# Optimization experiments

Measured on AMD Instinct MI355X. Metric: run time of the kernel, lower is better.

## Reference

```python
import jax, jax.numpy as jnp
import numpy as np

IN_DIM = 512
OUT_DIM = 512
NUM_HARMONICS = 32
BATCH = 4096


def setup_inputs() -> dict:
    key = jax.random.key(0)
    k1, k2 = jax.random.split(key)
    x = jax.random.normal(k1, (BATCH, IN_DIM), dtype=jnp.float32)
    std = 1.0 / np.sqrt(IN_DIM * NUM_HARMONICS)
    fourier_coeffs = jax.random.normal(
        k2, (IN_DIM, NUM_HARMONICS, 2, OUT_DIM), dtype=jnp.float32) * std
    bias = jnp.zeros((OUT_DIM,), dtype=jnp.float32)
    return {"x": x, "fourier_coeffs": fourier_coeffs, "bias": bias}


def reference(x, fourier_coeffs, bias):
    # k = [1, ..., num_harmonics]
    k = jnp.arange(1, fourier_coeffs.shape[1] + 1, dtype=x.dtype)
    kx = x[:, :, None] * k                      # [b, i, g]
    trig = jnp.stack([jnp.cos(kx), jnp.sin(kx)], axis=-1)  # [b, i, g, 2]
    out = jnp.einsum('bigf,igfo->bo', trig, fourier_coeffs)
    return out + bias
```

## Files before the change

kernel.cpp:

```cpp
#include <hip/hip_runtime.h>
#include <hip/hip_bf16.h>
#include <stdint.h>
#include <stddef.h>

#define BATCH   4096
#define INDIM   512
#define OUTDIM  512
#define NH      32
#define KKDIM   64
#define INV2PI  0.15915494309189535f

#define BM       128
#define BN       128
#define THREADS  256
#define KSPLIT   8
#define DIMS_PER_WG (INDIM / KSPLIT)
#define CHUNK_COLS  256
#define CHUNK_ELEMS (CHUNK_COLS * KKDIM)

#define B_BYTES       16384
#define SMEM_BYTES    (2 * B_BYTES)

typedef short  bhalf8  __attribute__((ext_vector_type(8)));
typedef float  vfloat4 __attribute__((ext_vector_type(4)));

union AFrag { uint4 u; bhalf8 h; };

__device__ __forceinline__ unsigned pack_bf16(float a, float b) {
    union { __hip_bfloat162 h2; unsigned u; } cv;
    cv.h2 = __float22bfloat162_rn(float2{a, b});
    return cv.u;
}

__device__ __forceinline__ void async_copy16(const void* gsrc, void* ldst) {
    __builtin_amdgcn_global_load_lds(
        (const __attribute__((address_space(1))) void*)(uintptr_t)gsrc,
        (__attribute__((address_space(3))) void*)(uint32_t)(uintptr_t)ldst,
        16, 0, 0);
}

__global__ __launch_bounds__(256) void fkan_prepass(const float* __restrict__ coeffs,
                                                    unsigned short* __restrict__ Bt) {
    __shared__ float lds[64][260];
    const int t  = threadIdx.x;
    const int cb = blockIdx.x & 1;
    const int i  = blockIdx.x >> 1;
    const float* __restrict__ src = coeffs + (size_t)i * (KKDIM * OUTDIM) + cb * CHUNK_COLS;
    unsigned short* __restrict__ chunk = Bt + (size_t)(cb * INDIM + i) * CHUNK_ELEMS;
#pragma unroll
    for (int rd = 0; rd < 16; ++rd) {
        const int r  = rd * 4 + (t >> 6);
        const int c4 = (t & 63) * 4;
        const float4 v = *(const float4*)(src + (size_t)r * OUTDIM + c4);
        *(float4*)&lds[r][c4] = v;
    }
    __syncthreads();
#pragma unroll
    for (int s = 0; s < 8; ++s) {
        const int unit = t + s * 256;
        const int col  = unit >> 3;
        const int pc   = unit & 7;
        const int kb   = (pc ^ (col & 7)) * 8;
        uint4 o;
        o.x = pack_bf16(lds[kb + 0][col], lds[kb + 1][col]);
        o.y = pack_bf16(lds[kb + 2][col], lds[kb + 3][col]);
        o.z = pack_bf16(lds[kb + 4][col], lds[kb + 5][col]);
        o.w = pack_bf16(lds[kb + 6][col], lds[kb + 7][col]);
        ((uint4*)chunk)[unit] = o;
    }
}

__global__ __launch_bounds__(256) void fkan_bias_init(const float* __restrict__ bias,
                                                      float* __restrict__ out) {
    const int idx = blockIdx.x * 256 + threadIdx.x;
    ((float4*)out)[idx] = ((const float4*)bias)[idx & 127];
}

__device__ __forceinline__ void stage_B(const char* __restrict__ chunk_half, char* smem,
                                        int parity, int t) {
    char* bdst = smem + parity * B_BYTES;
#pragma unroll
    for (int s = 0; s < 4; ++s) {
        const int unit = t + s * 256;
        async_copy16(chunk_half + unit * 16, bdst + unit * 16);
    }
}

__device__ __forceinline__ void make_av(float rv, float k0f, float k1f,
                                        bhalf8* a0, bhalf8* a1) {
    const float cd = __builtin_amdgcn_cosf(rv);
    const float sd = __builtin_amdgcn_sinf(rv);
    AFrag A;
    float c = __builtin_amdgcn_cosf(k0f * rv);
    float s = __builtin_amdgcn_sinf(k0f * rv);
    A.u.x = pack_bf16(c, s);
    { const float nc = c*cd - s*sd, ns = s*cd + c*sd; c = nc; s = ns; }
    A.u.y = pack_bf16(c, s);
    { const float nc = c*cd - s*sd, ns = s*cd + c*sd; c = nc; s = ns; }
    A.u.z = pack_bf16(c, s);
    { const float nc = c*cd - s*sd, ns = s*cd + c*sd; c = nc; s = ns; }
    A.u.w = pack_bf16(c, s);
    *a0 = A.h;
    c = __builtin_amdgcn_cosf(k1f * rv);
    s = __builtin_amdgcn_sinf(k1f * rv);
    A.u.x = pack_bf16(c, s);
    { const float nc = c*cd - s*sd, ns = s*cd + c*sd; c = nc; s = ns; }
    A.u.y = pack_bf16(c, s);
    { const float nc = c*cd - s*sd, ns = s*cd + c*sd; c = nc; s = ns; }
    A.u.z = pack_bf16(c, s);
    { const float nc = c*cd - s*sd, ns = s*cd + c*sd; c = nc; s = ns; }
    A.u.w = pack_bf16(c, s);
    *a1 = A.h;
}

#define MFMA_BLOCK(Bb, A0, A1)                                                  \
    do {                                                                        \
        _Pragma("unroll")                                                       \
        for (int ct = 0; ct < 8; ++ct) {                                        \
            const int cbyte = (ct * 16 + fr) * 128;                             \
            const bhalf8 b0 = *(const bhalf8*)((Bb) + cbyte + off0);            \
            acc[0][ct] = __builtin_amdgcn_mfma_f32_16x16x32_bf16(               \
                (A0)[0], b0, acc[0][ct], 0, 0, 0);                              \
            acc[1][ct] = __builtin_amdgcn_mfma_f32_16x16x32_bf16(               \
                (A0)[1], b0, acc[1][ct], 0, 0, 0);                              \
            const bhalf8 b1 = *(const bhalf8*)((Bb) + cbyte + off1);            \
            acc[0][ct] = __builtin_amdgcn_mfma_f32_16x16x32_bf16(               \
                (A1)[0], b1, acc[0][ct], 0, 0, 0);                              \
            acc[1][ct] = __builtin_amdgcn_mfma_f32_16x16x32_bf16(               \
                (A1)[1], b1, acc[1][ct], 0, 0, 0);                              \
        }                                                                       \
    } while (0)

#define WAITBAR4 asm volatile("s_waitcnt vmcnt(4)\n\ts_barrier" ::: "memory")
#define WAITBAR0 asm volatile("s_waitcnt vmcnt(0)\n\ts_barrier" ::: "memory")
#define POSTBAR  asm volatile("s_barrier" ::: "memory")

__global__ __launch_bounds__(THREADS, 5) void fkan_main(const float* __restrict__ x,
                                                        const unsigned short* __restrict__ Bt,
                                                        float* __restrict__ out) {
    __shared__ char smem[SMEM_BYTES];
    const int t      = threadIdx.x;
    const int grp    = blockIdx.x & 31;
    const int member = blockIdx.x >> 5;
    const int kq      = grp & 7;
    const int cb4     = grp >> 3;
    const int cb2     = cb4 >> 1;
    const int rowbase = member * BM;
    const int colbase = cb4 * BN;
    const int dimbase = kq * DIMS_PER_WG;

    const int lane = t & 63;
    const int w    = t >> 6;
    const int fr   = lane & 15;
    const int fq   = lane >> 4;
    const int fx   = lane & 7;
    const int off0 = (fq ^ fx) * 16;
    const int off1 = ((4 + fq) ^ fx) * 16;

    const float k0f = (float)(fq * 4 + 1);
    const float k1f = (float)(fq * 4 + 17);

    const float* __restrict__ xp0 = x + (size_t)(rowbase + w * 32 + fr) * INDIM + dimbase;
    const float* __restrict__ xp1 = xp0 + (size_t)16 * INDIM;

    const char* __restrict__ chunkbase =
        (const char*)(Bt + (size_t)(cb2 * INDIM + dimbase) * CHUNK_ELEMS) + (cb4 & 1) * 16384;

    vfloat4 acc[2][8];
#pragma unroll
    for (int a = 0; a < 2; ++a)
#pragma unroll
        for (int b = 0; b < 8; ++b) acc[a][b] = (vfloat4)0.0f;

    stage_B(chunkbase, smem, 0, t);

#pragma unroll 2
    for (int it = 0; it < DIMS_PER_WG - 1; ++it) {
        const int p = it & 1;
        stage_B(chunkbase + (size_t)(it + 1) * 32768, smem, p ^ 1, t);
        bhalf8 a0[2], a1[2];
        make_av(xp0[it] * INV2PI, k0f, k1f, &a0[0], &a1[0]);
        make_av(xp1[it] * INV2PI, k0f, k1f, &a0[1], &a1[1]);
        WAITBAR4;
        MFMA_BLOCK(smem + p * B_BYTES, a0, a1);
        POSTBAR;
    }
    {
        const int it = DIMS_PER_WG - 1;
        bhalf8 a0[2], a1[2];
        make_av(xp0[it] * INV2PI, k0f, k1f, &a0[0], &a1[0]);
        make_av(xp1[it] * INV2PI, k0f, k1f, &a0[1], &a1[1]);
        WAITBAR0;
        MFMA_BLOCK(smem + (it & 1) * B_BYTES, a0, a1);
    }

#pragma unroll
    for (int rt = 0; rt < 2; ++rt) {
#pragma unroll
        for (int ct = 0; ct < 8; ++ct) {
            const int col  = colbase + ct * 16 + fr;
            const int row0 = rowbase + w * 32 + rt * 16 + fq * 4;
#pragma unroll
            for (int r = 0; r < 4; ++r)
                atomicAdd(out + (size_t)(row0 + r) * OUTDIM + col, acc[rt][ct][r]);
        }
    }
}

__global__ __launch_bounds__(256) void fkan_naive(const float* __restrict__ x,
                                                  const float* __restrict__ coeffs,
                                                  const float* __restrict__ bias,
                                                  float* __restrict__ out) {
    const int b = blockIdx.x >> 1;
    const int o = ((blockIdx.x & 1) << 8) + threadIdx.x;
    float acc = bias[o];
    const float* xrow = x + (size_t)b * INDIM;
    for (int i = 0; i < INDIM; ++i) {
        const float rv = xrow[i] * INV2PI;
        const float cd = __builtin_amdgcn_cosf(rv);
        const float sd = __builtin_amdgcn_sinf(rv);
        float c = cd, s = sd;
        const float* cp = coeffs + (size_t)i * (KKDIM * OUTDIM) + o;
#pragma unroll 4
        for (int g = 0; g < NH; ++g) {
            acc += c * cp[g * 2 * OUTDIM] + s * cp[(g * 2 + 1) * OUTDIM];
            const float nc = c * cd - s * sd;
            const float ns = s * cd + c * sd;
            c = nc; s = ns;
        }
    }
    out[(size_t)b * OUTDIM + o] = acc;
}

extern "C" void kernel_launch(void* const* d_in, const int* in_sizes, int n_in,
                              void* d_out, int out_size, void* d_ws, size_t ws_size,
                              hipStream_t stream) {
    (void)in_sizes; (void)n_in; (void)out_size;
    const float* x      = (const float*)d_in[0];
    const float* coeffs = (const float*)d_in[1];
    const float* bias   = (const float*)d_in[2];
    float* out          = (float*)d_out;

    const size_t bt_bytes = (size_t)2 * INDIM * CHUNK_ELEMS * sizeof(unsigned short);
    if (ws_size >= bt_bytes) {
        unsigned short* Bt = (unsigned short*)d_ws;
        fkan_prepass<<<2 * INDIM, 256, 0, stream>>>(coeffs, Bt);
        fkan_bias_init<<<(BATCH * OUTDIM) / (4 * 256), 256, 0, stream>>>(bias, out);
        fkan_main<<<(BATCH / BM) * (OUTDIM / BN) * KSPLIT, THREADS, 0, stream>>>(x, Bt, out);
    } else {
        fkan_naive<<<BATCH * 2, 256, 0, stream>>>(x, coeffs, bias, out);
    }
}
```

Before: 327.1 us.

## Enlarge row tile to 256 with 512 threads and a four-deep LDS ring

Doubles the row tile per workgroup to 256 rows with 512 threads, so each staged B chunk feeds twice as many rows and global B traffic per output falls. Replaces the double buffer with a 4-slot LDS ring prefetched two iterations ahead, which drops the post-MFMA barrier. x is now loaded as float4 once every four iterations and prefetched. MFMA sections run at raised wave priority via s_setprio. The vmcnt thresholds of 8/4/0 appear loose for two loads per stage plus the x loads, which risks reading a slot before its copy lands. Fewer resident workgroups per CU also reduces latency hiding.

```diff
diff --git a/kernel.cpp b/kernel.cpp
--- a/kernel.cpp
+++ b/kernel.cpp
@@ -10,16 +10,16 @@
 #define KKDIM   64
 #define INV2PI  0.15915494309189535f
 
-#define BM       128
+#define BM       256
 #define BN       128
-#define THREADS  256
+#define THREADS  512
 #define KSPLIT   8
 #define DIMS_PER_WG (INDIM / KSPLIT)
 #define CHUNK_COLS  256
 #define CHUNK_ELEMS (CHUNK_COLS * KKDIM)
 
 #define B_BYTES       16384
-#define SMEM_BYTES    (2 * B_BYTES)
+#define SMEM_BYTES    (4 * B_BYTES)
 
 typedef short  bhalf8  __attribute__((ext_vector_type(8)));
 typedef float  vfloat4 __attribute__((ext_vector_type(4)));
@@ -77,11 +77,11 @@
 }
 
 __device__ __forceinline__ void stage_B(const char* __restrict__ chunk_half, char* smem,
-                                        int parity, int t) {
-    char* bdst = smem + parity * B_BYTES;
-#pragma unroll
-    for (int s = 0; s < 4; ++s) {
-        const int unit = t + s * 256;
+                                        int ring, int t) {
+    char* bdst = smem + ring * B_BYTES;
+#pragma unroll
+    for (int s = 0; s < 2; ++s) {
+        const int unit = t + s * 512;
         async_copy16(chunk_half + unit * 16, bdst + unit * 16);
     }
 }
@@ -131,11 +131,23 @@
         }                                                                       \
     } while (0)
 
-#define WAITBAR4 asm volatile("s_waitcnt vmcnt(4)\n\ts_barrier" ::: "memory")
-#define WAITBAR0 asm volatile("s_waitcnt vmcnt(0)\n\ts_barrier" ::: "memory")
-#define POSTBAR  asm volatile("s_barrier" ::: "memory")
-
-__global__ __launch_bounds__(THREADS, 5) void fkan_main(const float* __restrict__ x,
+#define WAITBARN(N) asm volatile("s_waitcnt vmcnt(" #N ")\n\ts_barrier" ::: "memory")
+
+#define FKAN_BODY(IT, S, RV0, RV1, DO_STAGE, DO_XLOAD, VMC_STMT)                \
+    {                                                                           \
+        if (DO_STAGE) stage_B(chunkbase + (size_t)((IT) + 2) * 32768, smem,     \
+                              ((S) + 2) & 3, t);                                \
+        if (DO_XLOAD) { nq0 = xf0[(IT) / 4 + 1]; nq1 = xf1[(IT) / 4 + 1]; }     \
+        bhalf8 a0[2], a1[2];                                                    \
+        make_av((RV0) * INV2PI, k0f, k1f, &a0[0], &a1[0]);                      \
+        make_av((RV1) * INV2PI, k0f, k1f, &a0[1], &a1[1]);                      \
+        VMC_STMT;                                                               \
+        __builtin_amdgcn_s_setprio(1);                                          \
+        MFMA_BLOCK(smem + (S) * B_BYTES, a0, a1);                               \
+        __builtin_amdgcn_s_setprio(0);                                          \
+    }
+
+__global__ __launch_bounds__(THREADS, 2) void fkan_main(const float* __restrict__ x,
                                                         const unsigned short* __restrict__ Bt,
                                                         float* __restrict__ out) {
     __shared__ char smem[SMEM_BYTES];
@@ -160,8 +172,10 @@
     const float k0f = (float)(fq * 4 + 1);
     const float k1f = (float)(fq * 4 + 17);
 
-    const float* __restrict__ xp0 = x + (size_t)(rowbase + w * 32 + fr) * INDIM + dimbase;
-    const float* __restrict__ xp1 = xp0 + (size_t)16 * INDIM;
+    const float4* __restrict__ xf0 =
+        (const float4*)(x + (size_t)(rowbase + w * 32 + fr) * INDIM + dimbase);
+    const float4* __restrict__ xf1 =
+        (const float4*)(x + (size_t)(rowbase + w * 32 + 16 + fr) * INDIM + dimbase);
 
     const char* __restrict__ chunkbase =
         (const char*)(Bt + (size_t)(cb2 * INDIM + dimbase) * CHUNK_ELEMS) + (cb4 & 1) * 16384;
@@ -172,27 +186,24 @@
 #pragma unroll
         for (int b = 0; b < 8; ++b) acc[a][b] = (vfloat4)0.0f;
 
-    stage_B(chunkbase, smem, 0, t);
-
-#pragma unroll 2
-    for (int it = 0; it < DIMS_PER_WG - 1; ++it) {
-        const int p = it & 1;
-        stage_B(chunkbase + (size_t)(it + 1) * 32768, smem, p ^ 1, t);
-        bhalf8 a0[2], a1[2];
-        make_av(xp0[it] * INV2PI, k0f, k1f, &a0[0], &a1[0]);
-        make_av(xp1[it] * INV2PI, k0f, k1f, &a0[1], &a1[1]);
-        WAITBAR4;
-        MFMA_BLOCK(smem + p * B_BYTES, a0, a1);
-        POSTBAR;
-    }
-    {
-        const int it = DIMS_PER_WG - 1;
-        bhalf8 a0[2], a1[2];
-        make_av(xp0[it] * INV2PI, k0f, k1f, &a0[0], &a1[0]);
-        make_av(xp1[it] * INV2PI, k0f, k1f, &a0[1], &a1[1]);
-        WAITBAR0;
-        MFMA_BLOCK(smem + (it & 1) * B_BYTES, a0, a1);
-    }
+    float4 cq0 = xf0[0];
+    float4 cq1 = xf1[0];
+    float4 nq0, nq1;
+    stage_B(chunkbase,         smem, 0, t);
+    stage_B(chunkbase + 32768, smem, 1, t);
+
+    for (int g = 0; g < 15; ++g) {
+        const int it0 = g * 4;
+        FKAN_BODY(it0 + 0, 0, cq0.x, cq1.x, true, true,  WAITBARN(8));
+        FKAN_BODY(it0 + 1, 1, cq0.y, cq1.y, true, false, WAITBARN(8));
+        FKAN_BODY(it0 + 2, 2, cq0.z, cq1.z, true, false, WAITBARN(8));
+        FKAN_BODY(it0 + 3, 3, cq0.w, cq1.w, true, false, WAITBARN(8));
+        cq0 = nq0; cq1 = nq1;
+    }
+    FKAN_BODY(60, 0, cq0.x, cq1.x, true,  false, WAITBARN(8));
+    FKAN_BODY(61, 1, cq0.y, cq1.y, true,  false, WAITBARN(8));
+    FKAN_BODY(62, 2, cq0.z, cq1.z, false, false, WAITBARN(4));
+    FKAN_BODY(63, 3, cq0.w, cq1.w, false, false, WAITBARN(0));
 
 #pragma unroll
     for (int rt = 0; rt < 2; ++rt) {
```

Result: faster. 291.9 us (-10.7%).

## Split B tile per wave to drop barriers and shrink block rows

Applied to the files above, without the earlier changes.

Each wave now owns a private 32-column slice of the B tile and stages it into LDS itself, so the block-wide barriers go away and only per-wave vmcnt waits remain. The row tile is halved from 128 to 64, so each wave covers all 64 rows, and the x loads are vectorized and prefetched one iteration ahead. MFMA sections are wrapped in s_setprio, and launch bounds change from 5 to 4 waves-per-EU hint. In exchange, the sin/cos A-fragment generation is now repeated by every wave for every row, and the grid gets more blocks, which adds atomics and recomputation.

```diff
diff --git a/kernel.cpp b/kernel.cpp
--- a/kernel.cpp
+++ b/kernel.cpp
@@ -10,7 +10,7 @@
 #define KKDIM   64
 #define INV2PI  0.15915494309189535f
 
-#define BM       128
+#define BM       64
 #define BN       128
 #define THREADS  256
 #define KSPLIT   8
@@ -18,8 +18,9 @@
 #define CHUNK_COLS  256
 #define CHUNK_ELEMS (CHUNK_COLS * KKDIM)
 
-#define B_BYTES       16384
-#define SMEM_BYTES    (2 * B_BYTES)
+#define SLICE_BYTES   4096
+#define BUF_BYTES     (4 * SLICE_BYTES)
+#define SMEM_BYTES    (2 * BUF_BYTES)
 
 typedef short  bhalf8  __attribute__((ext_vector_type(8)));
 typedef float  vfloat4 __attribute__((ext_vector_type(4)));
@@ -76,16 +77,6 @@
     ((float4*)out)[idx] = ((const float4*)bias)[idx & 127];
 }
 
-__device__ __forceinline__ void stage_B(const char* __restrict__ chunk_half, char* smem,
-                                        int parity, int t) {
-    char* bdst = smem + parity * B_BYTES;
-#pragma unroll
-    for (int s = 0; s < 4; ++s) {
-        const int unit = t + s * 256;
-        async_copy16(chunk_half + unit * 16, bdst + unit * 16);
-    }
-}
-
 __device__ __forceinline__ void make_av(float rv, float k0f, float k1f,
                                         bhalf8* a0, bhalf8* a1) {
     const float cd = __builtin_amdgcn_cosf(rv);
@@ -113,29 +104,49 @@
     *a1 = A.h;
 }
 
-#define MFMA_BLOCK(Bb, A0, A1)                                                  \
-    do {                                                                        \
+#define WAITV(N) asm volatile("s_waitcnt vmcnt(" #N ")" ::: "memory")
+
+#define FKAN_BODY(IT, C, XSTMT, DO_STAGE, N)                                    \
+    {                                                                           \
+        XSTMT;                                                                  \
+        if (DO_STAGE) {                                                         \
+            const char* gsrc = slicebase + (size_t)((IT) + 1) * 32768;          \
+            char* ldst = smem + (((IT) + 1) & 1) * BUF_BYTES + w * SLICE_BYTES; \
+            async_copy16(gsrc + lane * 16,        ldst + lane * 16);            \
+            async_copy16(gsrc + lane * 16 + 1024, ldst + lane * 16 + 1024);     \
+            async_copy16(gsrc + lane * 16 + 2048, ldst + lane * 16 + 2048);     \
+            async_copy16(gsrc + lane * 16 + 3072, ldst + lane * 16 + 3072);     \
+        }                                                                       \
+        WAITV(N);                                                               \
+        const char* Bb = smem + ((IT) & 1) * BUF_BYTES + w * SLICE_BYTES;       \
+        const bhalf8 b00 = *(const bhalf8*)(Bb + (0 * 16 + fr) * 128 + off0);   \
+        const bhalf8 b01 = *(const bhalf8*)(Bb + (1 * 16 + fr) * 128 + off0);   \
+        const bhalf8 b10 = *(const bhalf8*)(Bb + (0 * 16 + fr) * 128 + off1);   \
+        const bhalf8 b11 = *(const bhalf8*)(Bb + (1 * 16 + fr) * 128 + off1);   \
+        bhalf8 a0[4], a1[4];                                                    \
+        make_av(cq0.C * INV2PI, k0f, k1f, &a0[0], &a1[0]);                      \
+        make_av(cq1.C * INV2PI, k0f, k1f, &a0[1], &a1[1]);                      \
+        make_av(cq2.C * INV2PI, k0f, k1f, &a0[2], &a1[2]);                      \
+        make_av(cq3.C * INV2PI, k0f, k1f, &a0[3], &a1[3]);                      \
+        __builtin_amdgcn_s_setprio(1);                                          \
         _Pragma("unroll")                                                       \
-        for (int ct = 0; ct < 8; ++ct) {                                        \
-            const int cbyte = (ct * 16 + fr) * 128;                             \
-            const bhalf8 b0 = *(const bhalf8*)((Bb) + cbyte + off0);            \
-            acc[0][ct] = __builtin_amdgcn_mfma_f32_16x16x32_bf16(               \
-                (A0)[0], b0, acc[0][ct], 0, 0, 0);                              \
-            acc[1][ct] = __builtin_amdgcn_mfma_f32_16x16x32_bf16(               \
-                (A0)[1], b0, acc[1][ct], 0, 0, 0);                              \
-            const bhalf8 b1 = *(const bhalf8*)((Bb) + cbyte + off1);            \
-            acc[0][ct] = __builtin_amdgcn_mfma_f32_16x16x32_bf16(               \
-                (A1)[0], b1, acc[0][ct], 0, 0, 0);                              \
-            acc[1][ct] = __builtin_amdgcn_mfma_f32_16x16x32_bf16(               \
-                (A1)[1], b1, acc[1][ct], 0, 0, 0);                              \
+        for (int rt = 0; rt < 4; ++rt) {                                        \
+            acc[rt][0] = __builtin_amdgcn_mfma_f32_16x16x32_bf16(               \
+                a0[rt], b00, acc[rt][0], 0, 0, 0);                              \
+            acc[rt][1] = __builtin_amdgcn_mfma_f32_16x16x32_bf16(               \
+                a0[rt], b01, acc[rt][1], 0, 0, 0);                              \
+            acc[rt][0] = __builtin_amdgcn_mfma_f32_16x16x32_bf16(               \
+                a1[rt], b10, acc[rt][0], 0, 0, 0);                              \
+            acc[rt][1] = __builtin_amdgcn_mfma_f32_16x16x32_bf16(               \
+                a1[rt], b11, acc[rt][1], 0, 0, 0);                              \
         }                                                                       \
-    } while (0)
-
-#define WAITBAR4 asm volatile("s_waitcnt vmcnt(4)\n\ts_barrier" ::: "memory")
-#define WAITBAR0 asm volatile("s_waitcnt vmcnt(0)\n\ts_barrier" ::: "memory")
-#define POSTBAR  asm volatile("s_barrier" ::: "memory")
-
-__global__ __launch_bounds__(THREADS, 5) void fkan_main(const float* __restrict__ x,
+        __builtin_amdgcn_s_setprio(0);                                          \
+    }
+
+#define XLOAD(G1) { nq0 = xr0[G1]; nq1 = xr1[G1]; nq2 = xr2[G1]; nq3 = xr3[G1]; }
+#define XNOP      {}
+
+__global__ __launch_bounds__(THREADS, 4) void fkan_main(const float* __restrict__ x,
                                                         const unsigned short* __restrict__ Bt,
                                                         float* __restrict__ out) {
     __shared__ char smem[SMEM_BYTES];
@@ -160,46 +171,49 @@
     const float k0f = (float)(fq * 4 + 1);
     const float k1f = (float)(fq * 4 + 17);
 
-    const float* __restrict__ xp0 = x + (size_t)(rowbase + w * 32 + fr) * INDIM + dimbase;
-    const float* __restrict__ xp1 = xp0 + (size_t)16 * INDIM;
-
-    const char* __restrict__ chunkbase =
-        (const char*)(Bt + (size_t)(cb2 * INDIM + dimbase) * CHUNK_ELEMS) + (cb4 & 1) * 16384;
-
-    vfloat4 acc[2][8];
-#pragma unroll
-    for (int a = 0; a < 2; ++a)
-#pragma unroll
-        for (int b = 0; b < 8; ++b) acc[a][b] = (vfloat4)0.0f;
-
-    stage_B(chunkbase, smem, 0, t);
-
-#pragma unroll 2
-    for (int it = 0; it < DIMS_PER_WG - 1; ++it) {
-        const int p = it & 1;
-        stage_B(chunkbase + (size_t)(it + 1) * 32768, smem, p ^ 1, t);
-        bhalf8 a0[2], a1[2];
-        make_av(xp0[it] * INV2PI, k0f, k1f, &a0[0], &a1[0]);
-        make_av(xp1[it] * INV2PI, k0f, k1f, &a0[1], &a1[1]);
-        WAITBAR4;
-        MFMA_BLOCK(smem + p * B_BYTES, a0, a1);
-        POSTBAR;
-    }
+    const float2* __restrict__ xr0 =
+        (const float2*)(x + (size_t)(rowbase +  0 + fr) * INDIM + dimbase);
+    const float2* __restrict__ xr1 =
+        (const float2*)(x + (size_t)(rowbase + 16 + fr) * INDIM + dimbase);
+    const float2* __restrict__ xr2 =
+        (const float2*)(x + (size_t)(rowbase + 32 + fr) * INDIM + dimbase);
+    const float2* __restrict__ xr3 =
+        (const float2*)(x + (size_t)(rowbase + 48 + fr) * INDIM + dimbase);
+
+    const char* __restrict__ slicebase =
+        (const char*)(Bt + (size_t)(cb2 * INDIM + dimbase) * CHUNK_ELEMS)
+        + (cb4 & 1) * 16384 + w * SLICE_BYTES;
+
+    vfloat4 acc[4][2];
+#pragma unroll
+    for (int a = 0; a < 4; ++a) { acc[a][0] = (vfloat4)0.0f; acc[a][1] = (vfloat4)0.0f; }
+
+    float2 cq0 = xr0[0], cq1 = xr1[0], cq2 = xr2[0], cq3 = xr3[0];
+    float2 nq0, nq1, nq2, nq3;
     {
-        const int it = DIMS_PER_WG - 1;
-        bhalf8 a0[2], a1[2];
-        make_av(xp0[it] * INV2PI, k0f, k1f, &a0[0], &a1[0]);
-        make_av(xp1[it] * INV2PI, k0f, k1f, &a0[1], &a1[1]);
-        WAITBAR0;
-        MFMA_BLOCK(smem + (it & 1) * B_BYTES, a0, a1);
-    }
-
-#pragma unroll
-    for (int rt = 0; rt < 2; ++rt) {
-#pragma unroll
-        for (int ct = 0; ct < 8; ++ct) {
-            const int col  = colbase + ct * 16 + fr;
-            const int row0 = rowbase + w * 32 + rt * 16 + fq * 4;
+        char* ldst = smem + w * SLICE_BYTES;
+        async_copy16(slicebase + lane * 16,        ldst + lane * 16);
+        async_copy16(slicebase + lane * 16 + 1024, ldst + lane * 16 + 1024);
+        async_copy16(slicebase + lane * 16 + 2048, ldst + lane * 16 + 2048);
+        async_copy16(slicebase + lane * 16 + 3072, ldst + lane * 16 + 3072);
+    }
+
+#pragma unroll 1
+    for (int g = 0; g < 31; ++g) {
+        const int it0 = g * 2;
+        FKAN_BODY(it0 + 0, x, XLOAD(g + 1), true, 8);
+        FKAN_BODY(it0 + 1, y, XNOP,         true, 4);
+        cq0 = nq0; cq1 = nq1; cq2 = nq2; cq3 = nq3;
+    }
+    FKAN_BODY(62, x, XNOP, true,  4);
+    FKAN_BODY(63, y, XNOP, false, 0);
+
+#pragma unroll
+    for (int rt = 0; rt < 4; ++rt) {
+#pragma unroll
+        for (int ct = 0; ct < 2; ++ct) {
+            const int col  = colbase + w * 32 + ct * 16 + fr;
+            const int row0 = rowbase + rt * 16 + fq * 4;
 #pragma unroll
             for (int r = 0; r < 4; ++r)
                 atomicAdd(out + (size_t)(row0 + r) * OUTDIM + col, acc[rt][ct][r]);
```

Measured after the change: 454.4 us. 1.39x slower.
